# Kernel tuning notes

Measured on AMD Instinct MI355X. Metric: run time of the kernel, lower is better.

## Reference

```python
import jax, jax.numpy as jnp
import numpy as np

B, QN, D_IN = 2, 2048, 1024
NDS = QN // 2
HEADS, DIM_HEAD = 16, 64
INNER = HEADS * DIM_HEAD  # 1024
D_OUT = 1024


def setup_inputs() -> dict:
    key = jax.random.key(0)
    ks = jax.random.split(key, 7)
    s = 0.02
    return {
        "unet_full": jax.random.normal(ks[0], (B, QN, D_IN), jnp.float32),
        "unet_downsampled": jax.random.normal(ks[1], (B, NDS, D_IN), jnp.float32),
        "Wq": jax.random.normal(ks[2], (D_IN, INNER), jnp.float32) * s,
        "Wk": jax.random.normal(ks[3], (D_IN, INNER), jnp.float32) * s,
        "Wv": jax.random.normal(ks[4], (D_IN, INNER), jnp.float32) * s,
        "Wo": jax.random.normal(ks[5], (INNER, D_OUT), jnp.float32) * s,
        "bo": jnp.zeros((D_OUT,), jnp.float32),
    }


def reference(unet_full, unet_downsampled, Wq, Wk, Wv, Wo, bo):
    # projections
    q = unet_full @ Wq                      # [B, QN, H*D]
    k = unet_downsampled @ Wk               # [B, NDS, H*D]
    v = unet_downsampled @ Wv
    # repeat kv along sequence dim (torch repeat(1,2,1) == tile twice on dim 1)
    k = jnp.concatenate([k, k], axis=1)     # [B, KVN=2*NDS, H*D]
    v = jnp.concatenate([v, v], axis=1)
    kvn = k.shape[1]
    # split heads
    q = q.reshape(B, QN, HEADS, DIM_HEAD)
    k = k.reshape(B, kvn, HEADS, DIM_HEAD)
    v = v.reshape(B, kvn, HEADS, DIM_HEAD)
    # banded mask: triu(diagonal=-2) keeps entries where j >= i - 2; log -> 0 allowed, -inf blocked
    i = jnp.arange(QN)[:, None]
    j = jnp.arange(kvn)[None, :]
    bias = jnp.where(j >= i - 2, 0.0, -jnp.inf).astype(q.dtype)  # [QN, KVN]
    scale = 1.0 / jnp.sqrt(jnp.asarray(DIM_HEAD, q.dtype))
    scores = jnp.einsum('bqhd,bkhd->bhqk', q, k) * scale + bias[None, None]
    attn = jax.nn.softmax(scores, axis=-1)
    out = jnp.einsum('bhqk,bkhd->bqhd', attn, v)  # [B, QN, H, D]
    out = out.reshape(B, QN, INNER)
    return out @ Wo + bo
```

## Files before the change

kernel.cpp:

```cpp
#include <hip/hip_runtime.h>

typedef __attribute__((ext_vector_type(8))) short short8;
typedef __attribute__((ext_vector_type(4))) short short4v;
typedef __attribute__((ext_vector_type(4))) float floatx4;
typedef __attribute__((ext_vector_type(4))) unsigned int uint4v;
typedef __attribute__((ext_vector_type(2))) unsigned int uint2v;

__device__ __forceinline__ unsigned short f2bf(float f) {
  unsigned u = __float_as_uint(f);
  u += 0x7FFFu + ((u >> 16) & 1u);
  return (unsigned short)(u >> 16);
}
__device__ __forceinline__ unsigned pack_bf2(float f0, float f1) {
  unsigned a = __float_as_uint(f0) + 0x8000u;
  unsigned b = __float_as_uint(f1) + 0x8000u;
  return __builtin_amdgcn_perm(b, a, 0x07060302u);
}
__device__ __forceinline__ void async16(const unsigned short* g, unsigned short* l) {
  __builtin_amdgcn_global_load_lds(
      (const __attribute__((address_space(1))) unsigned int*)g,
      (__attribute__((address_space(3))) unsigned int*)l, 16, 0, 0);
}

#define B_   2
#define QN_  2048
#define NDS_ 1024
#define H_   16
#define C_SC 0.18033688011f

__global__ __launch_bounds__(256) void prep(
    const float* __restrict__ Wq, const float* __restrict__ Wk,
    const float* __restrict__ Wv, const float* __restrict__ Wo,
    const float* __restrict__ full, unsigned short* __restrict__ WT,
    unsigned short* __restrict__ full_bf) {
  int bid = blockIdx.x;
  if (bid < 1024) {
    int z = bid >> 8, tile = bid & 255;
    const float* W = z == 0 ? Wq : z == 1 ? Wk : z == 2 ? Wv : Wo;
    unsigned short* out = WT + (size_t)z * (1u << 20);
    __shared__ unsigned short tilebuf[64][65];
    int bi = tile >> 4, bj = tile & 15;
    int c = threadIdx.x & 63, r0 = threadIdx.x >> 6;
#pragma unroll
    for (int i = 0; i < 64; i += 4)
      tilebuf[r0 + i][c] = f2bf(W[(size_t)(bi * 64 + r0 + i) * 1024 + bj * 64 + c]);
    __syncthreads();
#pragma unroll
    for (int i = 0; i < 64; i += 4)
      out[(size_t)(bj * 64 + r0 + i) * 1024 + bi * 64 + c] = tilebuf[c][r0 + i];
  } else {
    size_t idx = ((size_t)(bid - 1024) * 256 + threadIdx.x) * 8;
    floatx4 a = *(const floatx4*)(full + idx);
    floatx4 b = *(const floatx4*)(full + idx + 4);
    uint4v u = {pack_bf2(a[0], a[1]), pack_bf2(a[2], a[3]),
                pack_bf2(b[0], b[1]), pack_bf2(b[2], b[3])};
    *(uint4v*)(full_bf + idx) = u;
  }
}

__global__ __launch_bounds__(256) void gemm_qkv(
    const unsigned short* __restrict__ fullbf, const float* __restrict__ ds,
    const unsigned short* __restrict__ WT,
    unsigned short* __restrict__ Qb, unsigned short* __restrict__ Kb,
    unsigned short* __restrict__ Vt) {
  __shared__ __align__(16) unsigned short As[128 * 32];
  __shared__ __align__(16) unsigned short Bs[128 * 32];
  int t = threadIdx.x;
  int lane = t & 63, wave = t >> 6;
  int lrow = lane & 15, quad = lane >> 4;
  int by = blockIdx.y;
  int colBase = blockIdx.x * 128;
  int wr = (wave & 1) * 64, wc = (wave >> 1) * 64;
  int sw = (lrow >> 1) & 3;

  int sel = (by < 32) ? 0 : (by < 48 ? 1 : 2);
  const unsigned short* Wt = WT + (size_t)sel * (1u << 20);
  size_t arow0 = (sel == 0) ? (size_t)by * 128
                            : (size_t)(by - (sel == 1 ? 32 : 48)) * 128;

  floatx4 acc[4][4];
#pragma unroll
  for (int mi = 0; mi < 4; ++mi)
#pragma unroll
    for (int ni = 0; ni < 4; ++ni) acc[mi][ni] = (floatx4){0.f, 0.f, 0.f, 0.f};

  for (int k0 = 0; k0 < 1024; k0 += 32) {
    __syncthreads();
    if (sel == 0) {
#pragma unroll
      for (int it = 0; it < 2; ++it) {
        int linear = it * 256 + t;
        int row = linear >> 2;
        int qg = (linear & 3) ^ ((row >> 1) & 3);
        async16(fullbf + (arow0 + row) * 1024 + k0 + qg * 8, As + linear * 8);
      }
    } else {
#pragma unroll
      for (int it = 0; it < 2; ++it) {
        int linear = it * 256 + t;
        int row = linear >> 2;
        int qg = (linear & 3) ^ ((row >> 1) & 3);
        const float* p = ds + (arow0 + row) * 1024 + k0 + qg * 8;
        floatx4 x = *(const floatx4*)p, y = *(const floatx4*)(p + 4);
        uint4v u = {pack_bf2(x[0], x[1]), pack_bf2(x[2], x[3]),
                    pack_bf2(y[0], y[1]), pack_bf2(y[2], y[3])};
        *(uint4v*)&As[linear * 8] = u;
      }
    }
#pragma unroll
    for (int it = 0; it < 2; ++it) {
      int linear = it * 256 + t;
      int row = linear >> 2;
      int qg = (linear & 3) ^ ((row >> 1) & 3);
      async16(Wt + (size_t)(colBase + row) * 1024 + k0 + qg * 8, Bs + linear * 8);
    }
    __syncthreads();

    short8 af[4], bfr[4];
#pragma unroll
    for (int mi = 0; mi < 4; ++mi)
      af[mi] = *(const short8*)&As[(wr + mi * 16 + lrow) * 32 + (quad ^ sw) * 8];
#pragma unroll
    for (int ni = 0; ni < 4; ++ni)
      bfr[ni] = *(const short8*)&Bs[(wc + ni * 16 + lrow) * 32 + (quad ^ sw) * 8];
#pragma unroll
    for (int mi = 0; mi < 4; ++mi)
#pragma unroll
      for (int ni = 0; ni < 4; ++ni)
        acc[mi][ni] =
            __builtin_amdgcn_mfma_f32_16x16x32_bf16(af[mi], bfr[ni], acc[mi][ni], 0, 0, 0);
  }

#pragma unroll
  for (int mi = 0; mi < 4; ++mi)
#pragma unroll
    for (int ni = 0; ni < 4; ++ni) {
      int col = colBase + wc + ni * 16 + lrow;
      if (sel == 2) {
        size_t r0g = arow0 + wr + mi * 16 + quad * 4;
        size_t b = r0g >> 10, kv = r0g & 1023;
        short4v pk;
#pragma unroll
        for (int r = 0; r < 4; ++r) pk[r] = (short)f2bf(acc[mi][ni][r]);
        *(short4v*)&Vt[b * (1u << 20) + (size_t)col * 1024 + kv] = pk;
      } else {
        unsigned short* C = (sel == 0) ? Qb : Kb;
#pragma unroll
        for (int r = 0; r < 4; ++r) {
          size_t row = arow0 + wr + mi * 16 + quad * 4 + r;
          C[row * 1024 + col] = f2bf(acc[mi][ni][r]);
        }
      }
    }
}

#define PSTR 40
__global__ __launch_bounds__(256) void attn_kernel(
    const unsigned short* __restrict__ Q,
    const unsigned short* __restrict__ K,
    const unsigned short* __restrict__ V,
    unsigned short* __restrict__ O) {
  __shared__ __align__(16) unsigned short Ks[2][32 * 64];
  __shared__ __align__(16) unsigned short Vs[2][64 * 32];
  __shared__ __align__(16) unsigned short Pl[4][16 * PSTR];
  int t = threadIdx.x, lane = t & 63, wave = t >> 6;
  int lrow = lane & 15, quad = lane >> 4;
  int bh = blockIdx.y, b = bh >> 4, h = bh & 15;
  int q0 = blockIdx.x * 64, qtile = q0 + wave * 16;
  int swk = lrow & 7, swv = (lrow >> 1) & 3;

  const unsigned short* qp =
      Q + (size_t)(b * QN_ + qtile + lrow) * 1024 + h * 64 + quad * 8;
  short8 qb0 = *(const short8*)qp;
  short8 qb1 = *(const short8*)(qp + 32);

  int krow = t >> 3, kq = (t & 7) ^ (krow & 7);
  const unsigned short* ksrc =
      K + (size_t)(b * NDS_ + krow) * 1024 + h * 64 + kq * 8;
  int vrow = t >> 2, vq = (t & 3) ^ ((vrow >> 1) & 3);
  const unsigned short* vsrc =
      V + ((size_t)b * 1024 + h * 64 + vrow) * 1024 + vq * 8;

  int c0 = (q0 >= 1058) ? (((q0 - 1058) >> 5) + 1) : 0;
  async16(ksrc + (size_t)c0 * 32 * 1024, &Ks[0][t * 8]);
  async16(vsrc + c0 * 32, &Vs[0][t * 8]);
  const unsigned short* kpre = ksrc + (size_t)(c0 + 1) * 32 * 1024;
  const unsigned short* vpre = vsrc + (c0 + 1) * 32;

  floatx4 acc_o[4];
#pragma unroll
  for (int dt = 0; dt < 4; ++dt) acc_o[dt] = (floatx4){0.f, 0.f, 0.f, 0.f};
  float den0 = 0.f, den1 = 0.f;
  int t1 = qtile + lrow - 2, t2 = qtile + lrow - 1026;
  unsigned short* P = Pl[wave];
  int buf = 0;

  for (int c = c0; c < 32; ++c) {
    __syncthreads();
    if (c + 1 < 32) {
      async16(kpre, &Ks[buf ^ 1][t * 8]);
      async16(vpre, &Vs[buf ^ 1][t * 8]);
      kpre += 32 * 1024;
      vpre += 32;
    }
    int cb = c * 32;
    bool fast2 = (cb >= qtile + 13);
    bool fast1 = (cb <= qtile - 34) && (cb >= qtile - 1011);
    if (fast1 || fast2) {
      float bias = fast2 ? 1.f : 0.f;
#pragma unroll
      for (int nt = 0; nt < 2; ++nt) {
        const unsigned short* kb = &Ks[buf][(nt * 16 + lrow) * 64];
        short8 ka0 = *(const short8*)(kb + (quad ^ swk) * 8);
        short8 ka1 = *(const short8*)(kb + ((quad + 4) ^ swk) * 8);
        floatx4 z = (floatx4){0.f, 0.f, 0.f, 0.f};
        z = __builtin_amdgcn_mfma_f32_16x16x32_bf16(ka0, qb0, z, 0, 0, 0);
        z = __builtin_amdgcn_mfma_f32_16x16x32_bf16(ka1, qb1, z, 0, 0, 0);
        float p[4];
#pragma unroll
        for (int r = 0; r < 4; ++r) {
          p[r] = __builtin_amdgcn_exp2f(fmaf(z[r], C_SC, bias));
          if (nt == 0) den0 += p[r]; else den1 += p[r];
        }
        uint2v pw = {pack_bf2(p[0], p[1]), pack_bf2(p[2], p[3])};
        *(uint2v*)&P[lrow * PSTR + nt * 16 + quad * 4] = pw;
      }
    } else {
#pragma unroll
      for (int nt = 0; nt < 2; ++nt) {
        const unsigned short* kb = &Ks[buf][(nt * 16 + lrow) * 64];
        short8 ka0 = *(const short8*)(kb + (quad ^ swk) * 8);
        short8 ka1 = *(const short8*)(kb + ((quad + 4) ^ swk) * 8);
        floatx4 z = (floatx4){0.f, 0.f, 0.f, 0.f};
        z = __builtin_amdgcn_mfma_f32_16x16x32_bf16(ka0, qb0, z, 0, 0, 0);
        z = __builtin_amdgcn_mfma_f32_16x16x32_bf16(ka1, qb1, z, 0, 0, 0);
        float p[4];
#pragma unroll
        for (int r = 0; r < 4; ++r) {
          int j0 = cb + nt * 16 + quad * 4 + r;
          float m = (j0 >= t1 ? 1.f : 0.f) + (j0 >= t2 ? 1.f : 0.f);
          p[r] = m * __builtin_amdgcn_exp2f(z[r] * C_SC);
          if (nt == 0) den0 += p[r]; else den1 += p[r];
        }
        uint2v pw = {pack_bf2(p[0], p[1]), pack_bf2(p[2], p[3])};
        *(uint2v*)&P[lrow * PSTR + nt * 16 + quad * 4] = pw;
      }
    }
    short8 pa = *(const short8*)&P[lrow * PSTR + quad * 8];
#pragma unroll
    for (int dt = 0; dt < 4; ++dt) {
      short8 vf =
          *(const short8*)&Vs[buf][(dt * 16 + lrow) * 32 + (quad ^ swv) * 8];
      acc_o[dt] = __builtin_amdgcn_mfma_f32_16x16x32_bf16(pa, vf, acc_o[dt], 0, 0, 0);
    }
    buf ^= 1;
  }
  float denom = den0 + den1;
  denom += __shfl_xor(denom, 16);
  denom += __shfl_xor(denom, 32);
  float dd[4];
#pragma unroll
  for (int r = 0; r < 4; ++r) dd[r] = __shfl(denom, quad * 4 + r);
#pragma unroll
  for (int dt = 0; dt < 4; ++dt)
#pragma unroll
    for (int r = 0; r < 4; ++r) {
      int i = qtile + quad * 4 + r;
      int col = h * 64 + dt * 16 + lrow;
      O[(size_t)(b * QN_ + i) * 1024 + col] = f2bf(acc_o[dt][r] / dd[r]);
    }
}

__global__ __launch_bounds__(256) void gemm_o(
    const unsigned short* __restrict__ Ab, const unsigned short* __restrict__ WoT,
    const float* __restrict__ bo, float* __restrict__ out) {
  __shared__ __align__(16) unsigned short As[64 * 32];
  __shared__ __align__(16) unsigned short Bs[128 * 32];
  int t = threadIdx.x;
  int lane = t & 63, wave = t >> 6;
  int lrow = lane & 15, quad = lane >> 4;
  size_t rowBase = (size_t)blockIdx.y * 64;
  int colBase = blockIdx.x * 128;
  int wr = (wave & 1) * 32, wc = (wave >> 1) * 64;
  int sw = (lrow >> 1) & 3;

  floatx4 acc[2][4];
#pragma unroll
  for (int mi = 0; mi < 2; ++mi)
#pragma unroll
    for (int ni = 0; ni < 4; ++ni) acc[mi][ni] = (floatx4){0.f, 0.f, 0.f, 0.f};

  for (int k0 = 0; k0 < 1024; k0 += 32) {
    __syncthreads();
    {
      int row = t >> 2;
      int qg = (t & 3) ^ ((row >> 1) & 3);
      async16(Ab + (rowBase + row) * 1024 + k0 + qg * 8, As + t * 8);
    }
#pragma unroll
    for (int it = 0; it < 2; ++it) {
      int linear = it * 256 + t;
      int row = linear >> 2;
      int qg = (linear & 3) ^ ((row >> 1) & 3);
      async16(WoT + (size_t)(colBase + row) * 1024 + k0 + qg * 8, Bs + linear * 8);
    }
    __syncthreads();

    short8 af[2], bfr[4];
#pragma unroll
    for (int mi = 0; mi < 2; ++mi)
      af[mi] = *(const short8*)&As[(wr + mi * 16 + lrow) * 32 + (quad ^ sw) * 8];
#pragma unroll
    for (int ni = 0; ni < 4; ++ni)
      bfr[ni] = *(const short8*)&Bs[(wc + ni * 16 + lrow) * 32 + (quad ^ sw) * 8];
#pragma unroll
    for (int mi = 0; mi < 2; ++mi)
#pragma unroll
      for (int ni = 0; ni < 4; ++ni)
        acc[mi][ni] =
            __builtin_amdgcn_mfma_f32_16x16x32_bf16(af[mi], bfr[ni], acc[mi][ni], 0, 0, 0);
  }

#pragma unroll
  for (int mi = 0; mi < 2; ++mi)
#pragma unroll
    for (int ni = 0; ni < 4; ++ni) {
      int col = colBase + wc + ni * 16 + lrow;
      float badd = bo[col];
#pragma unroll
      for (int r = 0; r < 4; ++r) {
        size_t row = rowBase + wr + mi * 16 + quad * 4 + r;
        out[row * 1024 + col] = acc[mi][ni][r] + badd;
      }
    }
}

extern "C" void kernel_launch(void* const* d_in, const int* in_sizes, int n_in,
                              void* d_out, int out_size, void* d_ws, size_t ws_size,
                              hipStream_t stream) {
  const float* full = (const float*)d_in[0];
  const float* ds   = (const float*)d_in[1];
  const float* Wq   = (const float*)d_in[2];
  const float* Wk   = (const float*)d_in[3];
  const float* Wv   = (const float*)d_in[4];
  const float* Wo   = (const float*)d_in[5];
  const float* bo   = (const float*)d_in[6];
  float* out = (float*)d_out;

  unsigned short* ws = (unsigned short*)d_ws;
  unsigned short* Qb      = ws;
  unsigned short* Kb      = ws + (4u << 20);
  unsigned short* Vt      = ws + (6u << 20);
  unsigned short* Ab      = ws + (8u << 20);
  unsigned short* full_bf = Ab;
  unsigned short* WT      = ws + (12u << 20);
  unsigned short* WoT     = WT + 3u * (1u << 20);

  dim3 tb(256);
  prep<<<3072, tb, 0, stream>>>(Wq, Wk, Wv, Wo, full, WT, full_bf);
  gemm_qkv<<<dim3(8, 64), tb, 0, stream>>>(full_bf, ds, WT, Qb, Kb, Vt);
  attn_kernel<<<dim3(QN_ / 64, B_ * H_), tb, 0, stream>>>(Qb, Kb, Vt, Ab);
  gemm_o<<<dim3(8, 64), tb, 0, stream>>>(Ab, WoT, bo, out);
}
```

Baseline: 189.2 us.

## Fuse full-input bf16 conversion into QKV GEMM and double K-tile depth

Removes the separate conversion of unet_full to bf16 in the prep kernel. The QKV GEMM now reads the fp32 activations directly and converts them while staging into LDS. Both GEMMs also move from a K step of 32 to 64, with an 8-way XOR swizzle, so each barrier pair is followed by twice as many MFMAs. The trade-offs are synchronous fp32 loads on the Q path where async LDS loads were used before, and a larger LDS footprint per block.

```diff
diff --git a/kernel.cpp b/kernel.cpp
--- a/kernel.cpp
+++ b/kernel.cpp
@@ -31,50 +31,41 @@
 __global__ __launch_bounds__(256) void prep(
     const float* __restrict__ Wq, const float* __restrict__ Wk,
     const float* __restrict__ Wv, const float* __restrict__ Wo,
-    const float* __restrict__ full, unsigned short* __restrict__ WT,
-    unsigned short* __restrict__ full_bf) {
+    unsigned short* __restrict__ WT) {
   int bid = blockIdx.x;
-  if (bid < 1024) {
-    int z = bid >> 8, tile = bid & 255;
-    const float* W = z == 0 ? Wq : z == 1 ? Wk : z == 2 ? Wv : Wo;
-    unsigned short* out = WT + (size_t)z * (1u << 20);
-    __shared__ unsigned short tilebuf[64][65];
-    int bi = tile >> 4, bj = tile & 15;
-    int c = threadIdx.x & 63, r0 = threadIdx.x >> 6;
-#pragma unroll
-    for (int i = 0; i < 64; i += 4)
-      tilebuf[r0 + i][c] = f2bf(W[(size_t)(bi * 64 + r0 + i) * 1024 + bj * 64 + c]);
-    __syncthreads();
-#pragma unroll
-    for (int i = 0; i < 64; i += 4)
-      out[(size_t)(bj * 64 + r0 + i) * 1024 + bi * 64 + c] = tilebuf[c][r0 + i];
-  } else {
-    size_t idx = ((size_t)(bid - 1024) * 256 + threadIdx.x) * 8;
-    floatx4 a = *(const floatx4*)(full + idx);
-    floatx4 b = *(const floatx4*)(full + idx + 4);
-    uint4v u = {pack_bf2(a[0], a[1]), pack_bf2(a[2], a[3]),
-                pack_bf2(b[0], b[1]), pack_bf2(b[2], b[3])};
-    *(uint4v*)(full_bf + idx) = u;
-  }
+  int z = bid >> 8, tile = bid & 255;
+  const float* W = z == 0 ? Wq : z == 1 ? Wk : z == 2 ? Wv : Wo;
+  unsigned short* out = WT + (size_t)z * (1u << 20);
+  __shared__ unsigned short tilebuf[64][65];
+  int bi = tile >> 4, bj = tile & 15;
+  int c = threadIdx.x & 63, r0 = threadIdx.x >> 6;
+#pragma unroll
+  for (int i = 0; i < 64; i += 4)
+    tilebuf[r0 + i][c] = f2bf(W[(size_t)(bi * 64 + r0 + i) * 1024 + bj * 64 + c]);
+  __syncthreads();
+#pragma unroll
+  for (int i = 0; i < 64; i += 4)
+    out[(size_t)(bj * 64 + r0 + i) * 1024 + bi * 64 + c] = tilebuf[c][r0 + i];
 }
 
 __global__ __launch_bounds__(256) void gemm_qkv(
-    const unsigned short* __restrict__ fullbf, const float* __restrict__ ds,
+    const float* __restrict__ full, const float* __restrict__ ds,
     const unsigned short* __restrict__ WT,
     unsigned short* __restrict__ Qb, unsigned short* __restrict__ Kb,
     unsigned short* __restrict__ Vt) {
-  __shared__ __align__(16) unsigned short As[128 * 32];
-  __shared__ __align__(16) unsigned short Bs[128 * 32];
+  __shared__ __align__(16) unsigned short As[128 * 64];
+  __shared__ __align__(16) unsigned short Bs[128 * 64];
   int t = threadIdx.x;
   int lane = t & 63, wave = t >> 6;
   int lrow = lane & 15, quad = lane >> 4;
   int by = blockIdx.y;
   int colBase = blockIdx.x * 128;
   int wr = (wave & 1) * 64, wc = (wave >> 1) * 64;
-  int sw = (lrow >> 1) & 3;
+  int sw = lrow & 7;
 
   int sel = (by < 32) ? 0 : (by < 48 ? 1 : 2);
   const unsigned short* Wt = WT + (size_t)sel * (1u << 20);
+  const float* Afp = (sel == 0) ? full : ds;
   size_t arow0 = (sel == 0) ? (size_t)by * 128
                             : (size_t)(by - (sel == 1 ? 32 : 48)) * 128;
 
@@ -84,51 +75,39 @@
 #pragma unroll
     for (int ni = 0; ni < 4; ++ni) acc[mi][ni] = (floatx4){0.f, 0.f, 0.f, 0.f};
 
-  for (int k0 = 0; k0 < 1024; k0 += 32) {
-    __syncthreads();
-    if (sel == 0) {
-#pragma unroll
-      for (int it = 0; it < 2; ++it) {
-        int linear = it * 256 + t;
-        int row = linear >> 2;
-        int qg = (linear & 3) ^ ((row >> 1) & 3);
-        async16(fullbf + (arow0 + row) * 1024 + k0 + qg * 8, As + linear * 8);
-      }
-    } else {
-#pragma unroll
-      for (int it = 0; it < 2; ++it) {
-        int linear = it * 256 + t;
-        int row = linear >> 2;
-        int qg = (linear & 3) ^ ((row >> 1) & 3);
-        const float* p = ds + (arow0 + row) * 1024 + k0 + qg * 8;
-        floatx4 x = *(const floatx4*)p, y = *(const floatx4*)(p + 4);
-        uint4v u = {pack_bf2(x[0], x[1]), pack_bf2(x[2], x[3]),
-                    pack_bf2(y[0], y[1]), pack_bf2(y[2], y[3])};
-        *(uint4v*)&As[linear * 8] = u;
-      }
-    }
-#pragma unroll
-    for (int it = 0; it < 2; ++it) {
+  for (int k0 = 0; k0 < 1024; k0 += 64) {
+    __syncthreads();
+#pragma unroll
+    for (int it = 0; it < 4; ++it) {
       int linear = it * 256 + t;
-      int row = linear >> 2;
-      int qg = (linear & 3) ^ ((row >> 1) & 3);
-      async16(Wt + (size_t)(colBase + row) * 1024 + k0 + qg * 8, Bs + linear * 8);
-    }
-    __syncthreads();
-
-    short8 af[4], bfr[4];
-#pragma unroll
-    for (int mi = 0; mi < 4; ++mi)
-      af[mi] = *(const short8*)&As[(wr + mi * 16 + lrow) * 32 + (quad ^ sw) * 8];
-#pragma unroll
-    for (int ni = 0; ni < 4; ++ni)
-      bfr[ni] = *(const short8*)&Bs[(wc + ni * 16 + lrow) * 32 + (quad ^ sw) * 8];
-#pragma unroll
-    for (int mi = 0; mi < 4; ++mi)
+      int row = linear >> 3;
+      int cg = (linear & 7) ^ (row & 7);
+      const float* p = Afp + (arow0 + row) * 1024 + k0 + cg * 8;
+      floatx4 x = *(const floatx4*)p, y = *(const floatx4*)(p + 4);
+      uint4v u = {pack_bf2(x[0], x[1]), pack_bf2(x[2], x[3]),
+                  pack_bf2(y[0], y[1]), pack_bf2(y[2], y[3])};
+      *(uint4v*)&As[linear * 8] = u;
+      async16(Wt + (size_t)(colBase + row) * 1024 + k0 + cg * 8, Bs + linear * 8);
+    }
+    __syncthreads();
+
+#pragma unroll
+    for (int ks = 0; ks < 2; ++ks) {
+      int fc = ((ks * 4 + quad) ^ sw) * 8;
+      short8 af[4], bfr[4];
+#pragma unroll
+      for (int mi = 0; mi < 4; ++mi)
+        af[mi] = *(const short8*)&As[(wr + mi * 16 + lrow) * 64 + fc];
 #pragma unroll
       for (int ni = 0; ni < 4; ++ni)
-        acc[mi][ni] =
-            __builtin_amdgcn_mfma_f32_16x16x32_bf16(af[mi], bfr[ni], acc[mi][ni], 0, 0, 0);
+        bfr[ni] = *(const short8*)&Bs[(wc + ni * 16 + lrow) * 64 + fc];
+#pragma unroll
+      for (int mi = 0; mi < 4; ++mi)
+#pragma unroll
+        for (int ni = 0; ni < 4; ++ni)
+          acc[mi][ni] =
+              __builtin_amdgcn_mfma_f32_16x16x32_bf16(af[mi], bfr[ni], acc[mi][ni], 0, 0, 0);
+    }
   }
 
 #pragma unroll
@@ -274,15 +253,15 @@
 __global__ __launch_bounds__(256) void gemm_o(
     const unsigned short* __restrict__ Ab, const unsigned short* __restrict__ WoT,
     const float* __restrict__ bo, float* __restrict__ out) {
-  __shared__ __align__(16) unsigned short As[64 * 32];
-  __shared__ __align__(16) unsigned short Bs[128 * 32];
+  __shared__ __align__(16) unsigned short As[64 * 64];
+  __shared__ __align__(16) unsigned short Bs[128 * 64];
   int t = threadIdx.x;
   int lane = t & 63, wave = t >> 6;
   int lrow = lane & 15, quad = lane >> 4;
   size_t rowBase = (size_t)blockIdx.y * 64;
   int colBase = blockIdx.x * 128;
   int wr = (wave & 1) * 32, wc = (wave >> 1) * 64;
-  int sw = (lrow >> 1) & 3;
+  int sw = lrow & 7;
 
   floatx4 acc[2][4];
 #pragma unroll
@@ -290,35 +269,41 @@
 #pragma unroll
     for (int ni = 0; ni < 4; ++ni) acc[mi][ni] = (floatx4){0.f, 0.f, 0.f, 0.f};
 
-  for (int k0 = 0; k0 < 1024; k0 += 32) {
-    __syncthreads();
-    {
-      int row = t >> 2;
-      int qg = (t & 3) ^ ((row >> 1) & 3);
-      async16(Ab + (rowBase + row) * 1024 + k0 + qg * 8, As + t * 8);
-    }
+  for (int k0 = 0; k0 < 1024; k0 += 64) {
+    __syncthreads();
 #pragma unroll
     for (int it = 0; it < 2; ++it) {
       int linear = it * 256 + t;
-      int row = linear >> 2;
-      int qg = (linear & 3) ^ ((row >> 1) & 3);
-      async16(WoT + (size_t)(colBase + row) * 1024 + k0 + qg * 8, Bs + linear * 8);
-    }
-    __syncthreads();
-
-    short8 af[2], bfr[4];
-#pragma unroll
-    for (int mi = 0; mi < 2; ++mi)
-      af[mi] = *(const short8*)&As[(wr + mi * 16 + lrow) * 32 + (quad ^ sw) * 8];
-#pragma unroll
-    for (int ni = 0; ni < 4; ++ni)
-      bfr[ni] = *(const short8*)&Bs[(wc + ni * 16 + lrow) * 32 + (quad ^ sw) * 8];
-#pragma unroll
-    for (int mi = 0; mi < 2; ++mi)
+      int row = linear >> 3;
+      int cg = (linear & 7) ^ (row & 7);
+      async16(Ab + (rowBase + row) * 1024 + k0 + cg * 8, As + linear * 8);
+    }
+#pragma unroll
+    for (int it = 0; it < 4; ++it) {
+      int linear = it * 256 + t;
+      int row = linear >> 3;
+      int cg = (linear & 7) ^ (row & 7);
+      async16(WoT + (size_t)(colBase + row) * 1024 + k0 + cg * 8, Bs + linear * 8);
+    }
+    __syncthreads();
+
+#pragma unroll
+    for (int ks = 0; ks < 2; ++ks) {
+      int fc = ((ks * 4 + quad) ^ sw) * 8;
+      short8 af[2], bfr[4];
+#pragma unroll
+      for (int mi = 0; mi < 2; ++mi)
+        af[mi] = *(const short8*)&As[(wr + mi * 16 + lrow) * 64 + fc];
 #pragma unroll
       for (int ni = 0; ni < 4; ++ni)
-        acc[mi][ni] =
-            __builtin_amdgcn_mfma_f32_16x16x32_bf16(af[mi], bfr[ni], acc[mi][ni], 0, 0, 0);
+        bfr[ni] = *(const short8*)&Bs[(wc + ni * 16 + lrow) * 64 + fc];
+#pragma unroll
+      for (int mi = 0; mi < 2; ++mi)
+#pragma unroll
+        for (int ni = 0; ni < 4; ++ni)
+          acc[mi][ni] =
+              __builtin_amdgcn_mfma_f32_16x16x32_bf16(af[mi], bfr[ni], acc[mi][ni], 0, 0, 0);
+    }
   }
 
 #pragma unroll
@@ -348,17 +333,16 @@
   float* out = (float*)d_out;
 
   unsigned short* ws = (unsigned short*)d_ws;
-  unsigned short* Qb      = ws;
-  unsigned short* Kb      = ws + (4u << 20);
-  unsigned short* Vt      = ws + (6u << 20);
-  unsigned short* Ab      = ws + (8u << 20);
-  unsigned short* full_bf = Ab;
-  unsigned short* WT      = ws + (12u << 20);
-  unsigned short* WoT     = WT + 3u * (1u << 20);
+  unsigned short* Qb  = ws;
+  unsigned short* Kb  = ws + (4u << 20);
+  unsigned short* Vt  = ws + (6u << 20);
+  unsigned short* Ab  = ws + (8u << 20);
+  unsigned short* WT  = ws + (12u << 20);
+  unsigned short* WoT = WT + 3u * (1u << 20);
 
   dim3 tb(256);
-  prep<<<3072, tb, 0, stream>>>(Wq, Wk, Wv, Wo, full, WT, full_bf);
-  gemm_qkv<<<dim3(8, 64), tb, 0, stream>>>(full_bf, ds, WT, Qb, Kb, Vt);
+  prep<<<1024, tb, 0, stream>>>(Wq, Wk, Wv, Wo, WT);
+  gemm_qkv<<<dim3(8, 64), tb, 0, stream>>>(full, ds, WT, Qb, Kb, Vt);
   attn_kernel<<<dim3(QN_ / 64, B_ * H_), tb, 0, stream>>>(Qb, Kb, Vt, Ab);
   gemm_o<<<dim3(8, 64), tb, 0, stream>>>(Ab, WoT, bo, out);
 }
```

Measured after the change: 177.8 us. -6.0%, faster.
